# Kernel optimization log

Hardware: AMD Instinct MI355X
Metric: run time of the kernel (lower is better)

Reference implementation:

```python
import jax, jax.numpy as jnp
import numpy as np

EPS = 1e-5


def _bn_relu(x, gamma, beta, mean, var):
    # inference-mode BatchNorm2d followed by ReLU, fused elementwise
    inv = gamma / jnp.sqrt(var + EPS)
    return jax.nn.relu((x - mean[None, :, None, None]) * inv[None, :, None, None]
                       + beta[None, :, None, None])


def _conv1x1(x, w, groups):
    # NCHW/OIHW grouped 1x1 conv, stride 1
    return jax.lax.conv_general_dilated(x, w, window_strides=(1, 1), padding='VALID',
                                        feature_group_count=groups)


def _active_shift(x, shift):
    # Per-channel learned 2D shift with bilinear interpolation, zero padding.
    # x: (N,C,H,W), shift: (C,2) = (dy, dx)
    N, C, H, W = x.shape
    dy, dx = shift[:, 0], shift[:, 1]
    ys = jnp.arange(H, dtype=x.dtype)[None, :] + dy[:, None]  # (C,H)
    xs = jnp.arange(W, dtype=x.dtype)[None, :] + dx[:, None]  # (C,W)
    y0 = jnp.floor(ys)
    x0 = jnp.floor(xs)
    wy = (ys - y0)[:, :, None]  # (C,H,1) frac weight toward y0+1
    wx = (xs - x0)[:, None, :]  # (C,1,W)

    def corner(yi, xi):
        valid = (((yi >= 0) & (yi <= H - 1))[:, :, None]
                 & ((xi >= 0) & (xi <= W - 1))[:, None, :]).astype(x.dtype)  # (C,H,W)
        yc = jnp.clip(yi, 0, H - 1).astype(jnp.int32)
        xc = jnp.clip(xi, 0, W - 1).astype(jnp.int32)
        g = jnp.take_along_axis(x, yc[None, :, :, None], axis=2)
        g = jnp.take_along_axis(g, xc[None, :, None, :], axis=3)
        return g * valid[None]

    out = ((1 - wy) * (1 - wx))[None] * corner(y0, x0) \
        + ((1 - wy) * wx)[None] * corner(y0, x0 + 1) \
        + (wy * (1 - wx))[None] * corner(y0 + 1, x0) \
        + (wy * wx)[None] * corner(y0 + 1, x0 + 1)
    return out


def setup_inputs() -> dict:
    key = jax.random.key(0)
    ks = jax.random.split(key, 16)
    N, Cin, H, W = 32, 96, 56, 56
    planes = 96
    return {
        'x': jax.random.normal(ks[0], (N, Cin, H, W), jnp.float32),
        'prev_fmap': jax.random.normal(ks[1], (N, Cin, H, W), jnp.float32),
        'bn1_gamma': jax.random.uniform(ks[2], (2 * Cin,), jnp.float32, 0.5, 1.5),
        'bn1_beta': jax.random.normal(ks[3], (2 * Cin,), jnp.float32) * 0.1,
        'bn1_mean': jax.random.normal(ks[4], (2 * Cin,), jnp.float32) * 0.1,
        'bn1_var': jax.random.uniform(ks[5], (2 * Cin,), jnp.float32, 0.5, 1.5),
        'bn2_gamma': jax.random.uniform(ks[6], (planes,), jnp.float32, 0.5, 1.5),
        'bn2_beta': jax.random.normal(ks[7], (planes,), jnp.float32) * 0.1,
        'bn2_mean': jax.random.normal(ks[8], (planes,), jnp.float32) * 0.1,
        'bn2_var': jax.random.uniform(ks[9], (planes,), jnp.float32, 0.5, 1.5),
        'w1': jax.random.normal(ks[10], (planes, 2 * Cin // 2, 1, 1), jnp.float32) * 0.05,
        'w2': jax.random.normal(ks[11], (planes, planes // 3, 1, 1), jnp.float32) * 0.05,
        'shift': jax.random.uniform(ks[12], (planes, 2), jnp.float32, -1.0, 1.0),
    }


def reference(x, prev_fmap, bn1_gamma, bn1_beta, bn1_mean, bn1_var,
              bn2_gamma, bn2_beta, bn2_mean, bn2_var, w1, w2, shift):
    x0, x1 = jnp.split(x, 2, axis=1)
    f0, f1 = jnp.split(prev_fmap, 2, axis=1)
    fmap = jnp.concatenate((x0, f1, x1, f0), axis=1)  # (N, 2*in_planes, H, W)
    fmap = _conv1x1(_bn_relu(fmap, bn1_gamma, bn1_beta, bn1_mean, bn1_var), w1, groups=2)
    h = _active_shift(_bn_relu(fmap, bn2_gamma, bn2_beta, bn2_mean, bn2_var), shift)
    out = _conv1x1(h, w2, groups=3) + x  # stride=1, in_planes==planes -> identity shortcut
    return (out, fmap)
```

## Files before the change

kernel.cpp:

```cpp
#include <hip/hip_runtime.h>
#include <hip/hip_bf16.h>
#include <string.h>

#define WSC_OFF 4608
#define WS_W2F  4800
#define WS_P    6336

#define HW 3136
#define CC 96
#define NB 32

typedef __attribute__((ext_vector_type(8))) short short8;
typedef __attribute__((ext_vector_type(4))) float float4_;

__global__ __launch_bounds__(128) void precompute_k(
    const float* __restrict__ g1, const float* __restrict__ be1,
    const float* __restrict__ m1, const float* __restrict__ v1,
    const float* __restrict__ g2, const float* __restrict__ be2,
    const float* __restrict__ m2, const float* __restrict__ v2,
    const float* __restrict__ w1, const float* __restrict__ w2,
    const float* __restrict__ shift, float* __restrict__ ws) {
  const int t = blockIdx.x * 128 + threadIdx.x;
  if (t < 192) {
    float s = g1[t] / sqrtf(v1[t] + 1e-5f);
    float b = be1[t] - m1[t] * s;
    ws[WSC_OFF + t] = b / s;
  }
  if (t >= 192 && t < 288) {
    int c = t - 192;
    float s = g2[c] / sqrtf(v2[c] + 1e-5f);
    float b = be2[c] - m2[c] * s;
    float dy = shift[2 * c], dx = shift[2 * c + 1];
    float fy = floorf(dy), fx = floorf(dx);
    float wy = dy - fy, wx = dx - fx;
    float* pp = ws + WS_P + c * 8;
    pp[0] = s;
    pp[1] = b;
    pp[2] = (1.f - wy) * (1.f - wx);
    pp[3] = (1.f - wy) * wx;
    pp[4] = wy * (1.f - wx);
    pp[5] = wy * wx;
    pp[6] = __int_as_float((int)fy);
    pp[7] = __int_as_float((int)fx);
  }
  if (t < 1152) {
    const int lane = t & 63;
    const int gmk = t >> 6;
    const int k = gmk % 3;
    const int gm = gmk / 3;
    const int m = gm % 3;
    const int g = gm / 3;
    const int o = 16 * m + (lane & 15);
    const int ci0 = 32 * k + (lane >> 4) * 8;
    unsigned int pk[4];
    for (int jj = 0; jj < 4; ++jj) {
      unsigned short us[2];
      for (int h = 0; h < 2; ++h) {
        int ci = ci0 + 2 * jj + h;
        float s = g1[g * 96 + ci] / sqrtf(v1[g * 96 + ci] + 1e-5f);
        float w = w1[(g * 48 + o) * 96 + ci] * s;
        __hip_bfloat16 hb = __float2bfloat16(w);
        memcpy(&us[h], &hb, 2);
      }
      pk[jj] = (unsigned int)us[0] | ((unsigned int)us[1] << 16);
    }
    uint4 val;
    val.x = pk[0]; val.y = pk[1]; val.z = pk[2]; val.w = pk[3];
    ((uint4*)ws)[t] = val;
  } else if (t < 1536) {
    const int s2i = t - 1152;
    const int lane = s2i & 63;
    const int gm = s2i >> 6;
    const int m = gm & 1;
    const int G = gm >> 1;
    const int o = G * 32 + m * 16 + (lane & 15);
    const int k0 = (lane >> 4) * 8;
    unsigned int pk[4];
    for (int jj = 0; jj < 4; ++jj) {
      unsigned short us[2];
      for (int h = 0; h < 2; ++h) {
        __hip_bfloat16 hb = __float2bfloat16(w2[o * 32 + k0 + 2 * jj + h]);
        memcpy(&us[h], &hb, 2);
      }
      pk[jj] = (unsigned int)us[0] | ((unsigned int)us[1] << 16);
    }
    uint4 val;
    val.x = pk[0]; val.y = pk[1]; val.z = pk[2]; val.w = pk[3];
    ((uint4*)(ws + WS_W2F))[s2i] = val;
  }
}

__global__ __launch_bounds__(256) void k1_conv1(
    const float* __restrict__ x, const float* __restrict__ prev,
    const float* __restrict__ ws, float* __restrict__ fmap) {
  const int tid = threadIdx.x;
  const int lane = tid & 63;
  const int wv = tid >> 6;
  const int g = blockIdx.y;
  const int strip = (blockIdx.x & 7) * 98 + (blockIdx.x >> 3);
  const int q = lane >> 4;
  const int colL = lane & 15;

  short8 A[3][3];
  const short8* wf = (const short8*)ws;
#pragma unroll
  for (int m = 0; m < 3; ++m)
#pragma unroll
    for (int k = 0; k < 3; ++k)
      A[m][k] = wf[((g * 3 + m) * 3 + k) * 64 + lane];

  float c_[3][8];
#pragma unroll
  for (int k = 0; k < 3; ++k) {
    const float* cp = ws + WSC_OFF + g * 96 + 32 * k + 8 * q;
#pragma unroll
    for (int j = 0; j < 8; ++j) c_[k][j] = cp[j];
  }

#pragma unroll
  for (int t = 0; t < 2; ++t) {
    const int P = strip * 128 + wv * 32 + t * 16;
    const int n = P / HW;
    const int p = P - n * HW;
    const size_t nb = (size_t)n * CC * HW;
    const int col = p + colL;

    float4_ D[3] = {{0.f, 0.f, 0.f, 0.f}, {0.f, 0.f, 0.f, 0.f},
                    {0.f, 0.f, 0.f, 0.f}};

#pragma unroll
    for (int k = 0; k < 3; ++k) {
      const int ci0 = 32 * k + 8 * q;
      const float* src = (ci0 < 48)
          ? (x + nb + (size_t)(g * 48 + ci0) * HW + col)
          : (prev + nb + (size_t)((1 - g) * 48 + (ci0 - 48)) * HW + col);
      float a[8];
#pragma unroll
      for (int j = 0; j < 8; ++j) a[j] = src[(size_t)j * HW];
      short8 B;
#pragma unroll
      for (int j = 0; j < 8; ++j) {
        float f = fmaxf(a[j] + c_[k][j], 0.f);
        __hip_bfloat16 hb = __float2bfloat16(f);
        unsigned short us;
        memcpy(&us, &hb, 2);
        B[j] = (short)us;
      }
#pragma unroll
      for (int m = 0; m < 3; ++m)
        D[m] = __builtin_amdgcn_mfma_f32_16x16x32_bf16(A[m][k], B, D[m],
                                                       0, 0, 0);
    }

    float* fb = fmap + nb + (size_t)(g * 48) * HW + col;
#pragma unroll
    for (int m = 0; m < 3; ++m)
#pragma unroll
      for (int r = 0; r < 4; ++r)
        fb[(size_t)(16 * m + q * 4 + r) * HW] = D[m][r];
  }
}

__global__ __launch_bounds__(256) void k2_shift_conv2(
    const float* __restrict__ x, const float* __restrict__ fmap,
    const float* __restrict__ ws, float* __restrict__ out) {
  const int tid = threadIdx.x;
  const int G = blockIdx.y;
  const int lane = tid & 63;
  const int wv = tid >> 6;
  const int q = lane >> 4;
  const int colL = lane & 15;
  const int strip = (blockIdx.x & 7) * 49 + (blockIdx.x >> 3);

  short8 A0, A1;
  {
    const short8* wf2 = (const short8*)(ws + WS_W2F);
    A0 = wf2[(G * 2 + 0) * 64 + lane];
    A1 = wf2[(G * 2 + 1) * 64 + lane];
  }

  float s_[8], b_[8], w00_[8], w01_[8], w10_[8], w11_[8];
  int off_[8], ay_[8], ax_[8];
#pragma unroll
  for (int j = 0; j < 8; ++j) {
    const float* pp = ws + WS_P + (G * 32 + q * 8 + j) * 8;
    s_[j] = pp[0];
    b_[j] = pp[1];
    w00_[j] = pp[2];
    w01_[j] = pp[3];
    w10_[j] = pp[4];
    w11_[j] = pp[5];
    ay_[j] = __float_as_int(pp[6]);
    ax_[j] = __float_as_int(pp[7]);
    off_[j] = ay_[j] * 56 + ax_[j];
  }

  const int P0 = strip * 256 + wv * 64;
  const int n = P0 / HW;
  const int pw = P0 - n * HW;
  const int cb = n * CC + G * 32;
  const float* fb = fmap + (size_t)cb * HW;
  const float* xb = x + (size_t)cb * HW;
  float* ob = out + (size_t)cb * HW;

#pragma unroll
  for (int t = 0; t < 4; ++t) {
    const int p = pw + t * 16 + colL;
    const int y = p / 56;
    const int xx = p - y * 56;

    float xr0[4], xr1[4];
#pragma unroll
    for (int r = 0; r < 4; ++r) {
      xr0[r] = xb[(size_t)(q * 4 + r) * HW + p];
      xr1[r] = xb[(size_t)(16 + q * 4 + r) * HW + p];
    }

    short8 B;
#pragma unroll
    for (int j = 0; j < 8; ++j) {
      const int ci = q * 8 + j;
      const float* fc = fb + (size_t)ci * HW;
      const int to = p + off_[j];
      float f00 = fc[to];
      float f01 = fc[min(to + 1, HW - 1)];
      float f10 = fc[min(to + 56, HW - 1)];
      float f11 = fc[min(to + 57, HW - 1)];
      float q00 = fmaxf(fmaf(f00, s_[j], b_[j]), 0.f);
      float q01 = fmaxf(fmaf(f01, s_[j], b_[j]), 0.f);
      float q10 = fmaxf(fmaf(f10, s_[j], b_[j]), 0.f);
      float q11 = fmaxf(fmaf(f11, s_[j], b_[j]), 0.f);
      const int yq = y + ay_[j], xq = xx + ax_[j];
      const bool vy0 = yq >= 0, vy1 = yq <= 54;
      const bool vx0 = xq >= 0, vx1 = xq <= 54;
      float h = ((vy0 && vx0) ? w00_[j] : 0.f) * q00;
      h = fmaf(((vy0 && vx1) ? w01_[j] : 0.f), q01, h);
      h = fmaf(((vy1 && vx0) ? w10_[j] : 0.f), q10, h);
      h = fmaf(((vy1 && vx1) ? w11_[j] : 0.f), q11, h);
      __hip_bfloat16 hb = __float2bfloat16(h);
      unsigned short us;
      memcpy(&us, &hb, 2);
      B[j] = (short)us;
    }

    float4_ D0 = {0.f, 0.f, 0.f, 0.f};
    float4_ D1 = {0.f, 0.f, 0.f, 0.f};
    D0 = __builtin_amdgcn_mfma_f32_16x16x32_bf16(A0, B, D0, 0, 0, 0);
    D1 = __builtin_amdgcn_mfma_f32_16x16x32_bf16(A1, B, D1, 0, 0, 0);

#pragma unroll
    for (int r = 0; r < 4; ++r) {
      ob[(size_t)(q * 4 + r) * HW + p] = D0[r] + xr0[r];
      ob[(size_t)(16 + q * 4 + r) * HW + p] = D1[r] + xr1[r];
    }
  }
}

extern "C" void kernel_launch(void* const* d_in, const int* in_sizes, int n_in,
                              void* d_out, int out_size, void* d_ws, size_t ws_size,
                              hipStream_t stream) {
  const float* x     = (const float*)d_in[0];
  const float* prev  = (const float*)d_in[1];
  const float* g1    = (const float*)d_in[2];
  const float* be1   = (const float*)d_in[3];
  const float* m1    = (const float*)d_in[4];
  const float* v1    = (const float*)d_in[5];
  const float* g2    = (const float*)d_in[6];
  const float* be2   = (const float*)d_in[7];
  const float* m2    = (const float*)d_in[8];
  const float* v2    = (const float*)d_in[9];
  const float* w1    = (const float*)d_in[10];
  const float* w2    = (const float*)d_in[11];
  const float* shift = (const float*)d_in[12];

  float* out  = (float*)d_out;
  float* fmap = out + (size_t)NB * CC * HW;
  float* ws   = (float*)d_ws;

  precompute_k<<<12, 128, 0, stream>>>(g1, be1, m1, v1, g2, be2, m2, v2,
                                       w1, w2, shift, ws);
  k1_conv1<<<dim3(784, 2), 256, 0, stream>>>(x, prev, ws, fmap);
  k2_shift_conv2<<<dim3(392, 3), 256, 0, stream>>>(x, fmap, ws, out);
}
```

Before: 63.40 us.

## Double-buffer conv1 input loads over larger strips and add nontemporal hints

The conv1 kernel now handles 256 pixels per block (four 16-column tiles per wave) instead of 128, and launches half as many blocks. It software-pipelines the loads, fetching the next tile's activations into a register double-buffer while the current tile is converted and fed to MFMA. Nontemporal loads and stores are used for data read or written only once: the prev_fmap half in conv1, and the residual x read and the output write in the shift/conv2 kernel. The goal is to hide global memory latency and reduce cache pollution, at the cost of more registers per thread and fewer blocks, which may lower occupancy.

```diff
diff --git a/kernel.cpp b/kernel.cpp
--- a/kernel.cpp
+++ b/kernel.cpp
@@ -97,7 +97,7 @@
   const int lane = tid & 63;
   const int wv = tid >> 6;
   const int g = blockIdx.y;
-  const int strip = (blockIdx.x & 7) * 98 + (blockIdx.x >> 3);
+  const int strip = (blockIdx.x & 7) * 49 + (blockIdx.x >> 3);
   const int q = lane >> 4;
   const int colL = lane & 15;
 
@@ -117,30 +117,56 @@
     for (int j = 0; j < 8; ++j) c_[k][j] = cp[j];
   }
 
-#pragma unroll
-  for (int t = 0; t < 2; ++t) {
-    const int P = strip * 128 + wv * 32 + t * 16;
-    const int n = P / HW;
-    const int p = P - n * HW;
-    const size_t nb = (size_t)n * CC * HW;
-    const int col = p + colL;
-
+  const int P0 = strip * 256 + wv * 64;
+  const int n = P0 / HW;
+  const int pw = P0 - n * HW;
+  const size_t nb = (size_t)n * CC * HW;
+
+  const float* sb[3];
+#pragma unroll
+  for (int k = 0; k < 3; ++k) {
+    const int ci0 = 32 * k + 8 * q;
+    sb[k] = (ci0 < 48)
+        ? (x + nb + (size_t)(g * 48 + ci0) * HW)
+        : (prev + nb + (size_t)((1 - g) * 48 + (ci0 - 48)) * HW);
+  }
+  float* fb = fmap + nb + (size_t)(g * 48) * HW;
+
+  float ab[2][3][8];
+  {
+    const int c0 = pw + colL;
+#pragma unroll
+    for (int k = 0; k < 3; ++k)
+#pragma unroll
+      for (int j = 0; j < 8; ++j)
+        ab[0][k][j] = (k == 2)
+            ? __builtin_nontemporal_load(sb[k] + (size_t)j * HW + c0)
+            : sb[k][(size_t)j * HW + c0];
+  }
+
+#pragma unroll
+  for (int t = 0; t < 4; ++t) {
+    const int cur = t & 1;
+    if (t < 3) {
+      const int cn = pw + (t + 1) * 16 + colL;
+#pragma unroll
+      for (int k = 0; k < 3; ++k)
+#pragma unroll
+        for (int j = 0; j < 8; ++j)
+          ab[cur ^ 1][k][j] = (k == 2)
+              ? __builtin_nontemporal_load(sb[k] + (size_t)j * HW + cn)
+              : sb[k][(size_t)j * HW + cn];
+    }
+
+    const int col = pw + t * 16 + colL;
     float4_ D[3] = {{0.f, 0.f, 0.f, 0.f}, {0.f, 0.f, 0.f, 0.f},
                     {0.f, 0.f, 0.f, 0.f}};
-
 #pragma unroll
     for (int k = 0; k < 3; ++k) {
-      const int ci0 = 32 * k + 8 * q;
-      const float* src = (ci0 < 48)
-          ? (x + nb + (size_t)(g * 48 + ci0) * HW + col)
-          : (prev + nb + (size_t)((1 - g) * 48 + (ci0 - 48)) * HW + col);
-      float a[8];
-#pragma unroll
-      for (int j = 0; j < 8; ++j) a[j] = src[(size_t)j * HW];
       short8 B;
 #pragma unroll
       for (int j = 0; j < 8; ++j) {
-        float f = fmaxf(a[j] + c_[k][j], 0.f);
+        float f = fmaxf(ab[cur][k][j] + c_[k][j], 0.f);
         __hip_bfloat16 hb = __float2bfloat16(f);
         unsigned short us;
         memcpy(&us, &hb, 2);
@@ -152,12 +178,11 @@
                                                        0, 0, 0);
     }
 
-    float* fb = fmap + nb + (size_t)(g * 48) * HW + col;
 #pragma unroll
     for (int m = 0; m < 3; ++m)
 #pragma unroll
       for (int r = 0; r < 4; ++r)
-        fb[(size_t)(16 * m + q * 4 + r) * HW] = D[m][r];
+        fb[(size_t)(16 * m + q * 4 + r) * HW + col] = D[m][r];
   }
 }
 
@@ -212,8 +237,8 @@
     float xr0[4], xr1[4];
 #pragma unroll
     for (int r = 0; r < 4; ++r) {
-      xr0[r] = xb[(size_t)(q * 4 + r) * HW + p];
-      xr1[r] = xb[(size_t)(16 + q * 4 + r) * HW + p];
+      xr0[r] = __builtin_nontemporal_load(xb + (size_t)(q * 4 + r) * HW + p);
+      xr1[r] = __builtin_nontemporal_load(xb + (size_t)(16 + q * 4 + r) * HW + p);
     }
 
     short8 B;
@@ -250,8 +275,10 @@
 
 #pragma unroll
     for (int r = 0; r < 4; ++r) {
-      ob[(size_t)(q * 4 + r) * HW + p] = D0[r] + xr0[r];
-      ob[(size_t)(16 + q * 4 + r) * HW + p] = D1[r] + xr1[r];
+      __builtin_nontemporal_store(D0[r] + xr0[r],
+                                  ob + (size_t)(q * 4 + r) * HW + p);
+      __builtin_nontemporal_store(D1[r] + xr1[r],
+                                  ob + (size_t)(16 + q * 4 + r) * HW + p);
     }
   }
 }
@@ -279,6 +306,6 @@
 
   precompute_k<<<12, 128, 0, stream>>>(g1, be1, m1, v1, g2, be2, m2, v2,
                                        w1, w2, shift, ws);
-  k1_conv1<<<dim3(784, 2), 256, 0, stream>>>(x, prev, ws, fmap);
+  k1_conv1<<<dim3(392, 2), 256, 0, stream>>>(x, prev, ws, fmap);
   k2_shift_conv2<<<dim3(392, 3), 256, 0, stream>>>(x, fmap, ws, out);
 }
```

Result: slower. 82.51 us (+30.2%).

## Fuse conv1 and shift-conv2 into one kernel with halo recompute in LDS

Applied to the files above, without the earlier changes.

Merges the two main kernels into one 512-thread kernel per 128-pixel strip. Conv1 is computed for the strip plus a 64-pixel halo on each side, and the BN2+ReLU result is stored as bf16 in shared memory. The shift and conv2 stage then read their bilinear neighbours from LDS instead of re-reading fmap from global memory. This removes the global fmap read-back and one kernel launch, at the cost of recomputing conv1 on the halo (double the conv1 work) and a large LDS footprint (about 50KB) that limits occupancy.

```diff
diff --git a/kernel.cpp b/kernel.cpp
--- a/kernel.cpp
+++ b/kernel.cpp
@@ -9,6 +9,8 @@
 #define HW 3136
 #define CC 96
 #define NB 32
+#define NP 100352
+#define LSTR 262
 
 typedef __attribute__((ext_vector_type(8))) short short8;
 typedef __attribute__((ext_vector_type(4))) float float4_;
@@ -90,168 +92,157 @@
   }
 }
 
-__global__ __launch_bounds__(256) void k1_conv1(
+__global__ __launch_bounds__(512) void fused_k(
     const float* __restrict__ x, const float* __restrict__ prev,
-    const float* __restrict__ ws, float* __restrict__ fmap) {
+    const float* __restrict__ ws, float* __restrict__ fmap,
+    float* __restrict__ out) {
+  __shared__ unsigned short qlds[CC * LSTR];
+
   const int tid = threadIdx.x;
   const int lane = tid & 63;
   const int wv = tid >> 6;
-  const int g = blockIdx.y;
-  const int strip = (blockIdx.x & 7) * 98 + (blockIdx.x >> 3);
-  const int q = lane >> 4;
+  const int qq = lane >> 4;
   const int colL = lane & 15;
-
-  short8 A[3][3];
-  const short8* wf = (const short8*)ws;
-#pragma unroll
-  for (int m = 0; m < 3; ++m)
-#pragma unroll
-    for (int k = 0; k < 3; ++k)
-      A[m][k] = wf[((g * 3 + m) * 3 + k) * 64 + lane];
-
-  float c_[3][8];
-#pragma unroll
-  for (int k = 0; k < 3; ++k) {
-    const float* cp = ws + WSC_OFF + g * 96 + 32 * k + 8 * q;
-#pragma unroll
-    for (int j = 0; j < 8; ++j) c_[k][j] = cp[j];
-  }
-
-#pragma unroll
-  for (int t = 0; t < 2; ++t) {
-    const int P = strip * 128 + wv * 32 + t * 16;
+  const int blk = (blockIdx.x & 7) * 98 + (blockIdx.x >> 3);
+  const int P0 = blk * 128;
+
+  {
+    const int g = wv >> 2;
+    short8 A[3][3];
+    const short8* wf = (const short8*)ws;
+#pragma unroll
+    for (int m = 0; m < 3; ++m)
+#pragma unroll
+      for (int k = 0; k < 3; ++k)
+        A[m][k] = wf[((g * 3 + m) * 3 + k) * 64 + lane];
+
+    float c_[3][8];
+#pragma unroll
+    for (int k = 0; k < 3; ++k) {
+      const float* cp = ws + WSC_OFF + g * 96 + 32 * k + 8 * qq;
+#pragma unroll
+      for (int j = 0; j < 8; ++j) c_[k][j] = cp[j];
+    }
+    float s2r[3][4], b2r[3][4];
+#pragma unroll
+    for (int m = 0; m < 3; ++m)
+#pragma unroll
+      for (int r = 0; r < 4; ++r) {
+        const int ch = 48 * g + 16 * m + 4 * qq + r;
+        const float* pp = ws + WS_P + ch * 8;
+        s2r[m][r] = pp[0];
+        b2r[m][r] = pp[1];
+      }
+
+#pragma unroll
+    for (int t = 0; t < 4; ++t) {
+      const int lt = (wv & 3) * 4 + t;
+      const int Pt = P0 - 64 + lt * 16;
+      const int lpx = lt * 16 + colL;
+      if ((unsigned)Pt >= (unsigned)NP) {
+#pragma unroll
+        for (int m = 0; m < 3; ++m)
+#pragma unroll
+          for (int r = 0; r < 4; ++r)
+            qlds[(48 * g + 16 * m + 4 * qq + r) * LSTR + lpx] = 0;
+        continue;
+      }
+      const int P = Pt + colL;
+      const int n = P / HW;
+      const int p = P - n * HW;
+      const size_t nb = (size_t)n * CC * HW;
+
+      float4_ D[3] = {{0.f,0.f,0.f,0.f},{0.f,0.f,0.f,0.f},{0.f,0.f,0.f,0.f}};
+#pragma unroll
+      for (int k = 0; k < 3; ++k) {
+        const int ci0 = 32 * k + 8 * qq;
+        const float* src = (ci0 < 48)
+            ? (x + nb + (size_t)(g * 48 + ci0) * HW + p)
+            : (prev + nb + (size_t)((1 - g) * 48 + (ci0 - 48)) * HW + p);
+        short8 B;
+#pragma unroll
+        for (int j = 0; j < 8; ++j) {
+          float f = fmaxf(src[(size_t)j * HW] + c_[k][j], 0.f);
+          __hip_bfloat16 hb = __float2bfloat16(f);
+          unsigned short us; memcpy(&us, &hb, 2);
+          B[j] = (short)us;
+        }
+#pragma unroll
+        for (int m = 0; m < 3; ++m)
+          D[m] = __builtin_amdgcn_mfma_f32_16x16x32_bf16(A[m][k], B, D[m],
+                                                         0, 0, 0);
+      }
+      if (lt >= 4 && lt < 12) {
+        float* fb = fmap + nb + (size_t)(g * 48) * HW + p;
+#pragma unroll
+        for (int m = 0; m < 3; ++m)
+#pragma unroll
+          for (int r = 0; r < 4; ++r)
+            fb[(size_t)(16 * m + 4 * qq + r) * HW] = D[m][r];
+      }
+#pragma unroll
+      for (int m = 0; m < 3; ++m)
+#pragma unroll
+        for (int r = 0; r < 4; ++r) {
+          float qv = fmaxf(fmaf(D[m][r], s2r[m][r], b2r[m][r]), 0.f);
+          __hip_bfloat16 hb = __float2bfloat16(qv);
+          unsigned short us; memcpy(&us, &hb, 2);
+          qlds[(48 * g + 16 * m + 4 * qq + r) * LSTR + lpx] = us;
+        }
+    }
+  }
+  __syncthreads();
+
+  {
+    const int Lpx = 64 + wv * 16 + colL;
+    const int P = P0 + wv * 16 + colL;
     const int n = P / HW;
     const int p = P - n * HW;
-    const size_t nb = (size_t)n * CC * HW;
-    const int col = p + colL;
-
-    float4_ D[3] = {{0.f, 0.f, 0.f, 0.f}, {0.f, 0.f, 0.f, 0.f},
-                    {0.f, 0.f, 0.f, 0.f}};
-
-#pragma unroll
-    for (int k = 0; k < 3; ++k) {
-      const int ci0 = 32 * k + 8 * q;
-      const float* src = (ci0 < 48)
-          ? (x + nb + (size_t)(g * 48 + ci0) * HW + col)
-          : (prev + nb + (size_t)((1 - g) * 48 + (ci0 - 48)) * HW + col);
-      float a[8];
-#pragma unroll
-      for (int j = 0; j < 8; ++j) a[j] = src[(size_t)j * HW];
-      short8 B;
-#pragma unroll
-      for (int j = 0; j < 8; ++j) {
-        float f = fmaxf(a[j] + c_[k][j], 0.f);
-        __hip_bfloat16 hb = __float2bfloat16(f);
-        unsigned short us;
-        memcpy(&us, &hb, 2);
-        B[j] = (short)us;
-      }
-#pragma unroll
-      for (int m = 0; m < 3; ++m)
-        D[m] = __builtin_amdgcn_mfma_f32_16x16x32_bf16(A[m][k], B, D[m],
-                                                       0, 0, 0);
-    }
-
-    float* fb = fmap + nb + (size_t)(g * 48) * HW + col;
-#pragma unroll
-    for (int m = 0; m < 3; ++m)
-#pragma unroll
-      for (int r = 0; r < 4; ++r)
-        fb[(size_t)(16 * m + q * 4 + r) * HW] = D[m][r];
-  }
-}
-
-__global__ __launch_bounds__(256) void k2_shift_conv2(
-    const float* __restrict__ x, const float* __restrict__ fmap,
-    const float* __restrict__ ws, float* __restrict__ out) {
-  const int tid = threadIdx.x;
-  const int G = blockIdx.y;
-  const int lane = tid & 63;
-  const int wv = tid >> 6;
-  const int q = lane >> 4;
-  const int colL = lane & 15;
-  const int strip = (blockIdx.x & 7) * 49 + (blockIdx.x >> 3);
-
-  short8 A0, A1;
-  {
-    const short8* wf2 = (const short8*)(ws + WS_W2F);
-    A0 = wf2[(G * 2 + 0) * 64 + lane];
-    A1 = wf2[(G * 2 + 1) * 64 + lane];
-  }
-
-  float s_[8], b_[8], w00_[8], w01_[8], w10_[8], w11_[8];
-  int off_[8], ay_[8], ax_[8];
-#pragma unroll
-  for (int j = 0; j < 8; ++j) {
-    const float* pp = ws + WS_P + (G * 32 + q * 8 + j) * 8;
-    s_[j] = pp[0];
-    b_[j] = pp[1];
-    w00_[j] = pp[2];
-    w01_[j] = pp[3];
-    w10_[j] = pp[4];
-    w11_[j] = pp[5];
-    ay_[j] = __float_as_int(pp[6]);
-    ax_[j] = __float_as_int(pp[7]);
-    off_[j] = ay_[j] * 56 + ax_[j];
-  }
-
-  const int P0 = strip * 256 + wv * 64;
-  const int n = P0 / HW;
-  const int pw = P0 - n * HW;
-  const int cb = n * CC + G * 32;
-  const float* fb = fmap + (size_t)cb * HW;
-  const float* xb = x + (size_t)cb * HW;
-  float* ob = out + (size_t)cb * HW;
-
-#pragma unroll
-  for (int t = 0; t < 4; ++t) {
-    const int p = pw + t * 16 + colL;
     const int y = p / 56;
     const int xx = p - y * 56;
-
-    float xr0[4], xr1[4];
-#pragma unroll
-    for (int r = 0; r < 4; ++r) {
-      xr0[r] = xb[(size_t)(q * 4 + r) * HW + p];
-      xr1[r] = xb[(size_t)(16 + q * 4 + r) * HW + p];
-    }
-
-    short8 B;
-#pragma unroll
-    for (int j = 0; j < 8; ++j) {
-      const int ci = q * 8 + j;
-      const float* fc = fb + (size_t)ci * HW;
-      const int to = p + off_[j];
-      float f00 = fc[to];
-      float f01 = fc[min(to + 1, HW - 1)];
-      float f10 = fc[min(to + 56, HW - 1)];
-      float f11 = fc[min(to + 57, HW - 1)];
-      float q00 = fmaxf(fmaf(f00, s_[j], b_[j]), 0.f);
-      float q01 = fmaxf(fmaf(f01, s_[j], b_[j]), 0.f);
-      float q10 = fmaxf(fmaf(f10, s_[j], b_[j]), 0.f);
-      float q11 = fmaxf(fmaf(f11, s_[j], b_[j]), 0.f);
-      const int yq = y + ay_[j], xq = xx + ax_[j];
-      const bool vy0 = yq >= 0, vy1 = yq <= 54;
-      const bool vx0 = xq >= 0, vx1 = xq <= 54;
-      float h = ((vy0 && vx0) ? w00_[j] : 0.f) * q00;
-      h = fmaf(((vy0 && vx1) ? w01_[j] : 0.f), q01, h);
-      h = fmaf(((vy1 && vx0) ? w10_[j] : 0.f), q10, h);
-      h = fmaf(((vy1 && vx1) ? w11_[j] : 0.f), q11, h);
-      __hip_bfloat16 hb = __float2bfloat16(h);
-      unsigned short us;
-      memcpy(&us, &hb, 2);
-      B[j] = (short)us;
-    }
-
-    float4_ D0 = {0.f, 0.f, 0.f, 0.f};
-    float4_ D1 = {0.f, 0.f, 0.f, 0.f};
-    D0 = __builtin_amdgcn_mfma_f32_16x16x32_bf16(A0, B, D0, 0, 0, 0);
-    D1 = __builtin_amdgcn_mfma_f32_16x16x32_bf16(A1, B, D1, 0, 0, 0);
-
-#pragma unroll
-    for (int r = 0; r < 4; ++r) {
-      ob[(size_t)(q * 4 + r) * HW + p] = D0[r] + xr0[r];
-      ob[(size_t)(16 + q * 4 + r) * HW + p] = D1[r] + xr1[r];
+    const short8* wf2 = (const short8*)(ws + WS_W2F);
+
+#pragma unroll
+    for (int G = 0; G < 3; ++G) {
+      short8 A0 = wf2[(G * 2 + 0) * 64 + lane];
+      short8 A1 = wf2[(G * 2 + 1) * 64 + lane];
+      short8 B;
+#pragma unroll
+      for (int j = 0; j < 8; ++j) {
+        const int ch = G * 32 + 8 * qq + j;
+        const float* pp = ws + WS_P + ch * 8;
+        const float w00 = pp[2], w01 = pp[3], w10 = pp[4], w11 = pp[5];
+        const int ay = __float_as_int(pp[6]);
+        const int ax = __float_as_int(pp[7]);
+        const unsigned short* qc = qlds + ch * LSTR + (Lpx + ay * 56 + ax);
+        const int yq = y + ay, xq = xx + ax;
+        const bool vy0 = yq >= 0, vy1 = yq <= 54;
+        const bool vx0 = xq >= 0, vx1 = xq <= 54;
+        float f00 = (vy0 && vx0) ? __uint_as_float((unsigned)qc[0] << 16) : 0.f;
+        float f01 = (vy0 && vx1) ? __uint_as_float((unsigned)qc[1] << 16) : 0.f;
+        float f10 = (vy1 && vx0) ? __uint_as_float((unsigned)qc[56] << 16) : 0.f;
+        float f11 = (vy1 && vx1) ? __uint_as_float((unsigned)qc[57] << 16) : 0.f;
+        float h = w00 * f00;
+        h = fmaf(w01, f01, h);
+        h = fmaf(w10, f10, h);
+        h = fmaf(w11, f11, h);
+        __hip_bfloat16 hb = __float2bfloat16(h);
+        unsigned short us; memcpy(&us, &hb, 2);
+        B[j] = (short)us;
+      }
+      const int cb = n * CC + G * 32;
+      const float* xb = x + (size_t)cb * HW + p;
+      float* ob = out + (size_t)cb * HW + p;
+      float4_ D0 = {0.f,0.f,0.f,0.f};
+      float4_ D1 = {0.f,0.f,0.f,0.f};
+      D0 = __builtin_amdgcn_mfma_f32_16x16x32_bf16(A0, B, D0, 0, 0, 0);
+      D1 = __builtin_amdgcn_mfma_f32_16x16x32_bf16(A1, B, D1, 0, 0, 0);
+#pragma unroll
+      for (int r = 0; r < 4; ++r) {
+        ob[(size_t)(qq * 4 + r) * HW] = D0[r] + xb[(size_t)(qq * 4 + r) * HW];
+        ob[(size_t)(16 + qq * 4 + r) * HW] =
+            D1[r] + xb[(size_t)(16 + qq * 4 + r) * HW];
+      }
     }
   }
 }
@@ -279,6 +270,5 @@
 
   precompute_k<<<12, 128, 0, stream>>>(g1, be1, m1, v1, g2, be2, m2, v2,
                                        w1, w2, shift, ws);
-  k1_conv1<<<dim3(784, 2), 256, 0, stream>>>(x, prev, ws, fmap);
-  k2_shift_conv2<<<dim3(392, 3), 256, 0, stream>>>(x, fmap, ws, out);
+  fused_k<<<784, 512, 0, stream>>>(x, prev, ws, fmap, out);
 }
```

Measured after the change: 73.76 us. 16.3% more time.
